# Optimization experiments

Measured on AMD Instinct MI355X. Metric: run time of the kernel, lower is better.

## Reference

```python
import jax, jax.numpy as jnp
import numpy as np

B, S, H = 2, 1024, 4096
NH, DH, NKV = 32, 128, 2          # heads, head_dim, kv groups
ROT = DH // 2                      # 64: GLM rotates first half of head dim
GROUP = NH // NKV                  # 16 query heads per kv group
SCALE = DH ** -0.5


def glm_rope(x, pos):
    """GLM interleaved rotary on first ROT dims. x: [B,S,h,DH], pos: [B,S] int."""
    rot, rest = x[..., :ROT], x[..., ROT:]
    inv_freq = 1.0 / (10000.0 ** (jnp.arange(0, ROT, 2, dtype=jnp.float32) / ROT))  # [ROT/2]
    ang = pos.astype(jnp.float32)[:, :, None] * inv_freq[None, None, :]             # [B,S,ROT/2]
    cos = jnp.cos(ang)[:, :, None, :]
    sin = jnp.sin(ang)[:, :, None, :]
    x0, x1 = rot[..., 0::2], rot[..., 1::2]
    o0 = x0 * cos - x1 * sin
    o1 = x1 * cos + x0 * sin
    rot_out = jnp.stack([o0, o1], axis=-1).reshape(rot.shape)
    return jnp.concatenate([rot_out, rest], axis=-1)


def setup_inputs() -> dict:
    key = jax.random.key(0)
    k1, k2, k3, k4 = jax.random.split(key, 4)
    return {
        "hidden_states": jax.random.normal(k1, (B, S, H), jnp.float32) * 0.02,
        "position_ids": jnp.arange(B * S, dtype=jnp.int32).reshape(B, S) % S,
        "W_qkv": jax.random.normal(k2, (H, NH * DH + 2 * NKV * DH), jnp.float32) * 0.02,
        "b_qkv": jax.random.normal(k3, (NH * DH + 2 * NKV * DH,), jnp.float32) * 0.02,
        "W_dense": jax.random.normal(k4, (NH * DH, H), jnp.float32) * 0.02,
    }


def reference(hidden_states, position_ids, W_qkv, b_qkv, W_dense):
    qkv = hidden_states @ W_qkv + b_qkv                              # [B,S,4608]
    q = qkv[..., : NH * DH].reshape(B, S, NH, DH)
    k = qkv[..., NH * DH : NH * DH + NKV * DH].reshape(B, S, NKV, DH)
    v = qkv[..., NH * DH + NKV * DH :].reshape(B, S, NKV, DH)

    q = glm_rope(q, position_ids)
    k = glm_rope(k, position_ids)

    # GQA: expand kv groups to all heads
    k = jnp.repeat(k, GROUP, axis=2)                                 # [B,S,NH,DH]
    v = jnp.repeat(v, GROUP, axis=2)

    scores = jnp.einsum("bqhd,bkhd->bhqk", q, k) * SCALE             # [B,NH,S,S]
    causal = jnp.tril(jnp.ones((S, S), dtype=bool))
    scores = jnp.where(causal[None, None], scores, jnp.finfo(scores.dtype).min)
    probs = jax.nn.softmax(scores, axis=-1)
    ctx = jnp.einsum("bhqk,bkhd->bqhd", probs, v).reshape(B, S, NH * DH)
    return ctx @ W_dense                                             # [B,S,H]
```

## Files before the change

kernel.cpp:

```cpp
#include <hip/hip_runtime.h>

#define B_    2
#define S_    1024
#define H_    4096
#define NH_   32
#define DH_   128
#define NKV_  2
#define GROUP_ 16
#define ROT_  64
#define NQKV_ 4608
#define SCALE_ 0.08838834764831845f
#define KVB   64

typedef __attribute__((ext_vector_type(8))) short bf16x8;
typedef __attribute__((ext_vector_type(4))) float f32x4;

typedef __attribute__((address_space(1))) const void* gptr_t;
typedef __attribute__((address_space(3))) void* lptr_t;

__device__ __forceinline__ unsigned short f2bf(float f) {
    unsigned int u = __builtin_bit_cast(unsigned int, f);
    u += 0x7FFFu + ((u >> 16) & 1u);
    return (unsigned short)(u >> 16);
}
__device__ __forceinline__ unsigned int pack2bf(float a, float b) {
    return (unsigned int)f2bf(a) | ((unsigned int)f2bf(b) << 16);
}

__global__ void k_f32_to_bf16(const float* __restrict__ in,
                              unsigned short* __restrict__ out, int n4) {
    int i = blockIdx.x * blockDim.x + threadIdx.x;
    if (i >= n4) return;
    const float4 v = reinterpret_cast<const float4*>(in)[i];
    ushort4 o;
    o.x = f2bf(v.x); o.y = f2bf(v.y); o.z = f2bf(v.z); o.w = f2bf(v.w);
    reinterpret_cast<ushort4*>(out)[i] = o;
}

__global__ void k_transpose_bf16(const float* __restrict__ in,
                                 unsigned short* __restrict__ out,
                                 int K, int N) {
    __shared__ float tile[32][33];
    const int n0 = blockIdx.x * 32, k0 = blockIdx.y * 32;
    const int tx = threadIdx.x, ty = threadIdx.y;
    for (int j = ty; j < 32; j += 8)
        tile[j][tx] = in[(size_t)(k0 + j) * N + n0 + tx];
    __syncthreads();
    for (int j = ty; j < 32; j += 8)
        out[(size_t)(n0 + j) * K + k0 + tx] = f2bf(tile[tx][j]);
}

__global__ void k_rope_tab(const int* __restrict__ pos_ids,
                           float2* __restrict__ tab) {
    const int idx = blockIdx.x * blockDim.x + threadIdx.x;
    if (idx >= B_ * S_ * 32) return;
    const int t = idx >> 5, pr = idx & 31;
    const float freq = exp2f(-0.41524101186092f * (float)pr);
    float sn, cs;
    sincosf((float)pos_ids[t] * freq, &sn, &cs);
    tab[idx] = make_float2(cs, sn);
}

template<int MODE>
__global__ __launch_bounds__(256, 2) void k_gemm(
    const unsigned short* __restrict__ A,
    const unsigned short* __restrict__ Bt,
    const float* __restrict__ bias,
    float* __restrict__ Cf,
    const float2* __restrict__ ctab,
    unsigned short* __restrict__ Qh,
    unsigned short* __restrict__ Kh,
    unsigned short* __restrict__ Vt,
    int M, int N, int K)
{
    __shared__ __align__(16) char lds[2][32768];

    const int tid  = threadIdx.x;
    const int wave = tid >> 6, lane = tid & 63;
    const int lrow = lane & 15, lhi = lane >> 4;
    const int wm = (wave >> 1) * 64, wn = (wave & 1) * 64;
    const size_t a_row0 = (size_t)blockIdx.y * 128;
    const size_t b_col0 = (size_t)blockIdx.x * 128;

    const size_t strideK = (size_t)K * 2;
    const char* Asrc = (const char*)A + (a_row0 + (tid >> 3)) * strideK;
    const char* Bsrc = (const char*)Bt + (b_col0 + (tid >> 3)) * strideK;
    const int swz_src = ((tid & 7) * 16) ^ (((tid >> 3) & 7) << 4);
    const int dst_off = tid * 16;

    f32x4 acc[4][4] = {};
    const int nt = K >> 6;

    #pragma unroll
    for (int j = 0; j < 4; j++) {
        __builtin_amdgcn_global_load_lds(
            (gptr_t)(Asrc + (size_t)j * 32 * strideK + swz_src),
            (lptr_t)(lds[0] + j * 4096 + dst_off), 16, 0, 0);
        __builtin_amdgcn_global_load_lds(
            (gptr_t)(Bsrc + (size_t)j * 32 * strideK + swz_src),
            (lptr_t)(lds[0] + 16384 + j * 4096 + dst_off), 16, 0, 0);
    }

    int cur = 0;
    for (int t = 0; t < nt; t++) {
        if (t + 1 < nt) {
            const size_t kb = (size_t)(t + 1) * 128;
            #pragma unroll
            for (int j = 0; j < 4; j++) {
                __builtin_amdgcn_global_load_lds(
                    (gptr_t)(Asrc + (size_t)j * 32 * strideK + kb + swz_src),
                    (lptr_t)(lds[cur ^ 1] + j * 4096 + dst_off), 16, 0, 0);
                __builtin_amdgcn_global_load_lds(
                    (gptr_t)(Bsrc + (size_t)j * 32 * strideK + kb + swz_src),
                    (lptr_t)(lds[cur ^ 1] + 16384 + j * 4096 + dst_off), 16, 0, 0);
            }
            asm volatile("s_waitcnt vmcnt(8)" ::: "memory");
        } else {
            asm volatile("s_waitcnt vmcnt(0)" ::: "memory");
        }
        __builtin_amdgcn_s_barrier();

        const char* La = lds[cur];
        const char* Lb = lds[cur] + 16384;
        bf16x8 af[4][2], bfr[4][2];
        #pragma unroll
        for (int i = 0; i < 4; i++) {
            const int fr = wm + i * 16 + lrow;
            af[i][0] = *(const bf16x8*)(La + fr * 128 + ((lhi * 16) ^ ((fr & 7) << 4)));
            af[i][1] = *(const bf16x8*)(La + fr * 128 + ((64 + lhi * 16) ^ ((fr & 7) << 4)));
        }
        #pragma unroll
        for (int j = 0; j < 4; j++) {
            const int br = wn + j * 16 + lrow;
            bfr[j][0] = *(const bf16x8*)(Lb + br * 128 + ((lhi * 16) ^ ((br & 7) << 4)));
            bfr[j][1] = *(const bf16x8*)(Lb + br * 128 + ((64 + lhi * 16) ^ ((br & 7) << 4)));
        }
        #pragma unroll
        for (int i = 0; i < 4; i++)
            #pragma unroll
            for (int j = 0; j < 4; j++) {
                acc[i][j] = __builtin_amdgcn_mfma_f32_16x16x32_bf16(
                    af[i][0], bfr[j][0], acc[i][j], 0, 0, 0);
                acc[i][j] = __builtin_amdgcn_mfma_f32_16x16x32_bf16(
                    af[i][1], bfr[j][1], acc[i][j], 0, 0, 0);
            }
        __builtin_amdgcn_s_barrier();
        cur ^= 1;
    }

    if (MODE == 0) {
        #pragma unroll
        for (int i = 0; i < 4; i++)
            #pragma unroll
            for (int j = 0; j < 4; j++) {
                const size_t grow0 = a_row0 + wm + i * 16 + lhi * 4;
                const size_t gcol  = b_col0 + wn + j * 16 + lrow;
                const float bi = bias ? bias[gcol] : 0.f;
                #pragma unroll
                for (int r = 0; r < 4; r++)
                    Cf[(grow0 + r) * N + gcol] = acc[i][j][r] + bi;
            }
    } else {
        const int bx = (int)blockIdx.x;
        const size_t bb = a_row0 >> 10;
        if (bx >= 34) {
            const int g = bx - 34;
            #pragma unroll
            for (int i = 0; i < 4; i++)
                #pragma unroll
                for (int j = 0; j < 4; j++) {
                    const int dloc = wn + j * 16 + lrow;
                    const float bi = bias[b_col0 + dloc];
                    const size_t row0 = a_row0 + wm + i * 16 + lhi * 4;
                    unsigned short* dst =
                        Vt + ((bb * NKV_ + g) * DH_ + dloc) * S_ + (row0 & 1023);
                    *reinterpret_cast<uint2*>(dst) = make_uint2(
                        pack2bf(acc[i][j][0] + bi, acc[i][j][1] + bi),
                        pack2bf(acc[i][j][2] + bi, acc[i][j][3] + bi));
                }
        } else {
            unsigned short* lds_c = (unsigned short*)&lds[0][0];
            #pragma unroll
            for (int i = 0; i < 4; i++)
                #pragma unroll
                for (int j = 0; j < 4; j++) {
                    const int dloc = wn + j * 16 + lrow;
                    const float bi = bias[b_col0 + dloc];
                    const int rloc0 = wm + i * 16 + lhi * 4;
                    float v[4];
                    #pragma unroll
                    for (int r = 0; r < 4; r++) v[r] = acc[i][j][r] + bi;
                    if (dloc < 64) {
                        const int pr = dloc >> 1;
                        #pragma unroll
                        for (int r = 0; r < 4; r++) {
                            const float2 cs = ctab[(a_row0 + rloc0 + r) * 32 + pr];
                            const float partner = __shfl_xor(v[r], 1);
                            v[r] = (dloc & 1) ? (v[r] * cs.x + partner * cs.y)
                                              : (v[r] * cs.x - partner * cs.y);
                        }
                    }
                    #pragma unroll
                    for (int r = 0; r < 4; r++)
                        lds_c[(rloc0 + r) * 128 + dloc] = f2bf(v[r]);
                }
            __syncthreads();
            unsigned short* base = (bx < 32)
                ? Qh + ((bb * NH_ + bx) * S_ + (a_row0 & 1023)) * DH_
                : Kh + ((bb * NKV_ + (bx - 32)) * S_ + (a_row0 & 1023)) * DH_;
            const int off = tid * 64;
            #pragma unroll
            for (int c = 0; c < 8; c++)
                *reinterpret_cast<uint4*>(base + off + c * 8) =
                    *reinterpret_cast<const uint4*>(lds_c + off + c * 8);
        }
    }
}

__global__ __launch_bounds__(256) void k_attn(
    const unsigned short* __restrict__ Qh,
    const unsigned short* __restrict__ Kh,
    const unsigned short* __restrict__ Vt,
    unsigned short* __restrict__ ctx)
{
    __shared__ __align__(16) char lds_kt[2][16384];
    __shared__ __align__(16) char lds_vt[16384];
    __shared__ __align__(16) char lds_p[4][2048];

    const int tid  = threadIdx.x;
    const int wave = tid >> 6, lane = tid & 63;
    const int lrow = lane & 15, lhi = lane >> 4;
    char* myp = lds_p[wave];

    const int blk  = blockIdx.x;
    const int pair = blk & 7;
    const int h    = (blk >> 3) & 31;
    const int b    = blk >> 8;
    const int g    = h >> 4;

    const char* Kbase = (const char*)(Kh + (size_t)((b * NKV_ + g) * S_) * DH_);
    const char* Vbase = (const char*)(Vt + (size_t)((b * NKV_ + g) * DH_) * S_);

    const int kcol = lrow * 16;
    const int vrow_l = lane >> 3;
    const int vcol = (lane & 7) * 16;

    for (int half = 0; half < 2; half++) {
        const int qt = half ? (15 - pair) : pair;
        const int q0 = qt * 64 + wave * 16;
        const int ntiles = qt + 1;
        const int q_glob = q0 + lrow;

        #pragma unroll
        for (int i = 0; i < 4; i++) {
            const int ci = wave * 4 + i;
            const int r  = ci * 4 + lhi;
            __builtin_amdgcn_global_load_lds(
                (gptr_t)(Kbase + (size_t)r * 256 + (kcol ^ ((r & 7) << 4))),
                (lptr_t)(lds_kt[0] + ci * 1024), 16, 0, 0);
        }
        const unsigned short* Qp = Qh + ((size_t)((b * NH_ + h) * S_) + q0) * DH_;
        bf16x8 a_q[4];
        #pragma unroll
        for (int ks = 0; ks < 4; ks++)
            a_q[ks] = *(const bf16x8*)(Qp + (size_t)lrow * DH_ + ks * 32 + lhi * 8);
        asm volatile("s_waitcnt vmcnt(0)" ::: "memory");
        __builtin_amdgcn_s_barrier();

        float m_run = -1e30f, l_run = 0.f;
        f32x4 o_acc[8] = {};
        int cur = 0;

        for (int t = 0; t < ntiles; t++) {
            const bool has_next = (t + 1 < ntiles);
            #pragma unroll
            for (int i = 0; i < 4; i++) {
                const int ci = wave * 4 + i;
                const int r  = ci * 8 + vrow_l;
                __builtin_amdgcn_global_load_lds(
                    (gptr_t)(Vbase + (size_t)r * (S_ * 2) + t * (KVB * 2)
                             + (vcol ^ ((r & 7) << 4))),
                    (lptr_t)(lds_vt + ci * 1024), 16, 0, 0);
            }
            if (has_next) {
                const char* ksrc = Kbase + (size_t)(t + 1) * 16384;
                #pragma unroll
                for (int i = 0; i < 4; i++) {
                    const int ci = wave * 4 + i;
                    const int r  = ci * 4 + lhi;
                    __builtin_amdgcn_global_load_lds(
                        (gptr_t)(ksrc + (size_t)r * 256 + (kcol ^ ((r & 7) << 4))),
                        (lptr_t)(lds_kt[cur ^ 1] + ci * 1024), 16, 0, 0);
                }
            }
            f32x4 s_acc[4] = {};
            #pragma unroll
            for (int sub = 0; sub < 4; sub++) {
                const int r = sub * 16 + lrow;
                #pragma unroll
                for (int ks = 0; ks < 4; ks++) {
                    const bf16x8 a_k = *(const bf16x8*)(
                        lds_kt[cur] + r * 256 + ((ks * 64 + lhi * 16) ^ ((r & 7) << 4)));
                    s_acc[sub] = __builtin_amdgcn_mfma_f32_16x16x32_bf16(
                        a_k, a_q[ks], s_acc[sub], 0, 0, 0);
                }
            }
            float pv[16];
            float mx = -1e30f;
            if (!has_next) {
                #pragma unroll
                for (int sub = 0; sub < 4; sub++)
                    #pragma unroll
                    for (int r = 0; r < 4; r++) {
                        const int kvg = t * KVB + sub * 16 + lhi * 4 + r;
                        float sv = s_acc[sub][r] * SCALE_;
                        if (kvg > q_glob) sv = -1e30f;
                        pv[sub * 4 + r] = sv;
                        mx = fmaxf(mx, sv);
                    }
            } else {
                #pragma unroll
                for (int sub = 0; sub < 4; sub++)
                    #pragma unroll
                    for (int r = 0; r < 4; r++) {
                        const float sv = s_acc[sub][r] * SCALE_;
                        pv[sub * 4 + r] = sv;
                        mx = fmaxf(mx, sv);
                    }
            }
            mx = fmaxf(mx, __shfl_xor(mx, 16));
            mx = fmaxf(mx, __shfl_xor(mx, 32));
            const float mnew = fmaxf(m_run, mx);
            const float scale = __expf(m_run - mnew);
            m_run = mnew;
            float sm = 0.f;
            #pragma unroll
            for (int i = 0; i < 16; i++) {
                const float e = __expf(pv[i] - mnew);
                pv[i] = e;
                sm += e;
            }
            sm += __shfl_xor(sm, 16);
            sm += __shfl_xor(sm, 32);
            l_run = l_run * scale + sm;
            #pragma unroll
            for (int d = 0; d < 8; d++) {
                o_acc[d][0] *= scale; o_acc[d][1] *= scale;
                o_acc[d][2] *= scale; o_acc[d][3] *= scale;
            }
            #pragma unroll
            for (int sub = 0; sub < 4; sub++) {
                const int off = (lrow * 128 + sub * 32 + lhi * 8) ^ ((lrow & 7) << 4);
                *reinterpret_cast<uint2*>(myp + off) = make_uint2(
                    pack2bf(pv[sub * 4 + 0], pv[sub * 4 + 1]),
                    pack2bf(pv[sub * 4 + 2], pv[sub * 4 + 3]));
            }
            bf16x8 a_p[2];
            #pragma unroll
            for (int frag = 0; frag < 2; frag++) {
                const int off = (lrow * 128 + frag * 64 + lhi * 16) ^ ((lrow & 7) << 4);
                a_p[frag] = *reinterpret_cast<const bf16x8*>(myp + off);
            }
            if (has_next) asm volatile("s_waitcnt vmcnt(4)" ::: "memory");
            else          asm volatile("s_waitcnt vmcnt(0)" ::: "memory");
            __builtin_amdgcn_s_barrier();
            #pragma unroll
            for (int d = 0; d < 8; d++) {
                const int r = d * 16 + lrow;
                #pragma unroll
                for (int frag = 0; frag < 2; frag++) {
                    const bf16x8 a_v = *(const bf16x8*)(
                        lds_vt + r * 128 + ((frag * 64 + lhi * 16) ^ ((r & 7) << 4)));
                    o_acc[d] = __builtin_amdgcn_mfma_f32_16x16x32_bf16(
                        a_v, a_p[frag], o_acc[d], 0, 0, 0);
                }
            }
            asm volatile("s_waitcnt vmcnt(0)" ::: "memory");
            __builtin_amdgcn_s_barrier();
            cur ^= 1;
        }
        const float inv = 1.f / l_run;
        const size_t row = (size_t)b * S_ + q0 + lrow;
        #pragma unroll
        for (int d = 0; d < 8; d++) {
            unsigned short* dst = ctx + row * (NH_ * DH_) + h * DH_ + d * 16 + lhi * 4;
            *reinterpret_cast<uint2*>(dst) = make_uint2(
                pack2bf(o_acc[d][0] * inv, o_acc[d][1] * inv),
                pack2bf(o_acc[d][2] * inv, o_acc[d][3] * inv));
        }
    }
}

extern "C" void kernel_launch(void* const* d_in, const int* in_sizes, int n_in,
                              void* d_out, int out_size, void* d_ws, size_t ws_size,
                              hipStream_t stream)
{
    const float* hidden  = (const float*)d_in[0];
    const int*   pos_ids = (const int*)d_in[1];
    const float* W_qkv   = (const float*)d_in[2];
    const float* b_qkv   = (const float*)d_in[3];
    const float* W_dense = (const float*)d_in[4];
    float* out = (float*)d_out;

    char* ws = (char*)d_ws;
    unsigned short* Xbf = (unsigned short*)(ws);
    unsigned short* Wqt = (unsigned short*)(ws + 16777216);
    unsigned short* Wdt = (unsigned short*)(ws + 54525952);
    float2*         ctab= (float2*)        (ws + 88080384);
    unsigned short* Qh  = (unsigned short*)(ws + 125829120);
    unsigned short* Kh  = (unsigned short*)(ws + 142606336);
    unsigned short* Vt  = (unsigned short*)(ws + 143654912);
    unsigned short* Ctx = (unsigned short*)(ws + 144703488);

    const int M = B_ * S_;

    k_f32_to_bf16<<<(M * H_ / 4 + 255) / 256, 256, 0, stream>>>(hidden, Xbf, M * H_ / 4);
    k_rope_tab<<<(M * 32 + 255) / 256, 256, 0, stream>>>(pos_ids, ctab);
    dim3 tb(32, 8);
    k_transpose_bf16<<<dim3(NQKV_ / 32, H_ / 32), tb, 0, stream>>>(W_qkv, Wqt, H_, NQKV_);
    k_transpose_bf16<<<dim3(H_ / 32, H_ / 32), tb, 0, stream>>>(W_dense, Wdt, H_, H_);
    k_gemm<1><<<dim3(NQKV_ / 128, M / 128), 256, 0, stream>>>(
        Xbf, Wqt, b_qkv, nullptr, ctab, Qh, Kh, Vt, M, NQKV_, H_);
    k_attn<<<B_ * NH_ * 8, 256, 0, stream>>>(Qh, Kh, Vt, Ctx);
    k_gemm<0><<<dim3(H_ / 128, M / 128), 256, 0, stream>>>(
        Ctx, Wdt, nullptr, out, nullptr, nullptr, nullptr, nullptr, M, H_, H_);
}
```

Baseline: 294.4 us.

## Shrink GEMM tile to 64x128, remap blocks across XCDs, swizzle epilogue LDS

Both GEMMs now use 64x128 output tiles instead of 128x128. The grid becomes 1D, with a block-id remap that groups consecutive tiles by XCD (blockIdx & 7), and occupancy is raised to 3 blocks per CU with smaller LDS buffers. The aim is more blocks and better load balance across the 256 CUs, plus better L2 locality per XCD. The QK epilogue staging buffer also gains an XOR swizzle to cut LDS bank conflicts. The trade-off is lower arithmetic intensity per tile, since each B fragment is reused over half as many rows.

Result: slower. 318.5 us (+8.2%).

```diff
diff --git a/kernel.cpp b/kernel.cpp
--- a/kernel.cpp
+++ b/kernel.cpp
@@ -62,7 +62,7 @@
 }
 
 template<int MODE>
-__global__ __launch_bounds__(256, 2) void k_gemm(
+__global__ __launch_bounds__(256, 3) void k_gemm(
     const unsigned short* __restrict__ A,
     const unsigned short* __restrict__ Bt,
     const float* __restrict__ bias,
@@ -73,14 +73,19 @@
     unsigned short* __restrict__ Vt,
     int M, int N, int K)
 {
-    __shared__ __align__(16) char lds[2][32768];
+    __shared__ __align__(16) char lds[2][24576];
 
     const int tid  = threadIdx.x;
     const int wave = tid >> 6, lane = tid & 63;
     const int lrow = lane & 15, lhi = lane >> 4;
-    const int wm = (wave >> 1) * 64, wn = (wave & 1) * 64;
-    const size_t a_row0 = (size_t)blockIdx.y * 128;
-    const size_t b_col0 = (size_t)blockIdx.x * 128;
+    const int wm = (wave >> 1) * 32, wn = (wave & 1) * 64;
+
+    const int cpx = gridDim.x >> 3;
+    const int Lid = ((int)blockIdx.x & 7) * cpx + ((int)blockIdx.x >> 3);
+    const int bx = Lid >> 5;
+    const int by = Lid & 31;
+    const size_t a_row0 = (size_t)by * 64;
+    const size_t b_col0 = (size_t)bx * 128;
 
     const size_t strideK = (size_t)K * 2;
     const char* Asrc = (const char*)A + (a_row0 + (tid >> 3)) * strideK;
@@ -88,43 +93,45 @@
     const int swz_src = ((tid & 7) * 16) ^ (((tid >> 3) & 7) << 4);
     const int dst_off = tid * 16;
 
-    f32x4 acc[4][4] = {};
+    f32x4 acc[2][4] = {};
     const int nt = K >> 6;
 
     #pragma unroll
-    for (int j = 0; j < 4; j++) {
+    for (int j = 0; j < 2; j++)
         __builtin_amdgcn_global_load_lds(
             (gptr_t)(Asrc + (size_t)j * 32 * strideK + swz_src),
             (lptr_t)(lds[0] + j * 4096 + dst_off), 16, 0, 0);
+    #pragma unroll
+    for (int j = 0; j < 4; j++)
         __builtin_amdgcn_global_load_lds(
             (gptr_t)(Bsrc + (size_t)j * 32 * strideK + swz_src),
-            (lptr_t)(lds[0] + 16384 + j * 4096 + dst_off), 16, 0, 0);
-    }
+            (lptr_t)(lds[0] + 8192 + j * 4096 + dst_off), 16, 0, 0);
 
     int cur = 0;
     for (int t = 0; t < nt; t++) {
         if (t + 1 < nt) {
             const size_t kb = (size_t)(t + 1) * 128;
             #pragma unroll
-            for (int j = 0; j < 4; j++) {
+            for (int j = 0; j < 2; j++)
                 __builtin_amdgcn_global_load_lds(
                     (gptr_t)(Asrc + (size_t)j * 32 * strideK + kb + swz_src),
                     (lptr_t)(lds[cur ^ 1] + j * 4096 + dst_off), 16, 0, 0);
+            #pragma unroll
+            for (int j = 0; j < 4; j++)
                 __builtin_amdgcn_global_load_lds(
                     (gptr_t)(Bsrc + (size_t)j * 32 * strideK + kb + swz_src),
-                    (lptr_t)(lds[cur ^ 1] + 16384 + j * 4096 + dst_off), 16, 0, 0);
-            }
-            asm volatile("s_waitcnt vmcnt(8)" ::: "memory");
+                    (lptr_t)(lds[cur ^ 1] + 8192 + j * 4096 + dst_off), 16, 0, 0);
+            asm volatile("s_waitcnt vmcnt(6)" ::: "memory");
         } else {
             asm volatile("s_waitcnt vmcnt(0)" ::: "memory");
         }
         __builtin_amdgcn_s_barrier();
 
         const char* La = lds[cur];
-        const char* Lb = lds[cur] + 16384;
-        bf16x8 af[4][2], bfr[4][2];
-        #pragma unroll
-        for (int i = 0; i < 4; i++) {
+        const char* Lb = lds[cur] + 8192;
+        bf16x8 af[2][2], bfr[4][2];
+        #pragma unroll
+        for (int i = 0; i < 2; i++) {
             const int fr = wm + i * 16 + lrow;
             af[i][0] = *(const bf16x8*)(La + fr * 128 + ((lhi * 16) ^ ((fr & 7) << 4)));
             af[i][1] = *(const bf16x8*)(La + fr * 128 + ((64 + lhi * 16) ^ ((fr & 7) << 4)));
@@ -136,7 +143,7 @@
             bfr[j][1] = *(const bf16x8*)(Lb + br * 128 + ((64 + lhi * 16) ^ ((br & 7) << 4)));
         }
         #pragma unroll
-        for (int i = 0; i < 4; i++)
+        for (int i = 0; i < 2; i++)
             #pragma unroll
             for (int j = 0; j < 4; j++) {
                 acc[i][j] = __builtin_amdgcn_mfma_f32_16x16x32_bf16(
@@ -150,7 +157,7 @@
 
     if (MODE == 0) {
         #pragma unroll
-        for (int i = 0; i < 4; i++)
+        for (int i = 0; i < 2; i++)
             #pragma unroll
             for (int j = 0; j < 4; j++) {
                 const size_t grow0 = a_row0 + wm + i * 16 + lhi * 4;
@@ -161,12 +168,11 @@
                     Cf[(grow0 + r) * N + gcol] = acc[i][j][r] + bi;
             }
     } else {
-        const int bx = (int)blockIdx.x;
         const size_t bb = a_row0 >> 10;
         if (bx >= 34) {
             const int g = bx - 34;
             #pragma unroll
-            for (int i = 0; i < 4; i++)
+            for (int i = 0; i < 2; i++)
                 #pragma unroll
                 for (int j = 0; j < 4; j++) {
                     const int dloc = wn + j * 16 + lrow;
@@ -179,9 +185,9 @@
                         pack2bf(acc[i][j][2] + bi, acc[i][j][3] + bi));
                 }
         } else {
-            unsigned short* lds_c = (unsigned short*)&lds[0][0];
-            #pragma unroll
-            for (int i = 0; i < 4; i++)
+            char* lc = &lds[0][0];
+            #pragma unroll
+            for (int i = 0; i < 2; i++)
                 #pragma unroll
                 for (int j = 0; j < 4; j++) {
                     const int dloc = wn + j * 16 + lrow;
@@ -201,18 +207,24 @@
                         }
                     }
                     #pragma unroll
-                    for (int r = 0; r < 4; r++)
-                        lds_c[(rloc0 + r) * 128 + dloc] = f2bf(v[r]);
+                    for (int r = 0; r < 4; r++) {
+                        const int row = rloc0 + r;
+                        *(unsigned short*)(lc + row * 256 +
+                            ((dloc * 2) ^ ((row & 7) << 4))) = f2bf(v[r]);
+                    }
                 }
             __syncthreads();
             unsigned short* base = (bx < 32)
                 ? Qh + ((bb * NH_ + bx) * S_ + (a_row0 & 1023)) * DH_
                 : Kh + ((bb * NKV_ + (bx - 32)) * S_ + (a_row0 & 1023)) * DH_;
-            const int off = tid * 64;
-            #pragma unroll
-            for (int c = 0; c < 8; c++)
-                *reinterpret_cast<uint4*>(base + off + c * 8) =
-                    *reinterpret_cast<const uint4*>(lds_c + off + c * 8);
+            #pragma unroll
+            for (int c = 0; c < 4; c++) {
+                const int lin = tid * 64 + c * 16;
+                const int row = lin >> 8;
+                const int col = (lin & 255) ^ ((row & 7) << 4);
+                *reinterpret_cast<uint4*>((char*)base + lin) =
+                    *reinterpret_cast<const uint4*>(lc + row * 256 + col);
+            }
         }
     }
 }
@@ -419,9 +431,9 @@
     dim3 tb(32, 8);
     k_transpose_bf16<<<dim3(NQKV_ / 32, H_ / 32), tb, 0, stream>>>(W_qkv, Wqt, H_, NQKV_);
     k_transpose_bf16<<<dim3(H_ / 32, H_ / 32), tb, 0, stream>>>(W_dense, Wdt, H_, H_);
-    k_gemm<1><<<dim3(NQKV_ / 128, M / 128), 256, 0, stream>>>(
+    k_gemm<1><<<dim3((NQKV_ / 128) * (M / 64)), 256, 0, stream>>>(
         Xbf, Wqt, b_qkv, nullptr, ctab, Qh, Kh, Vt, M, NQKV_, H_);
     k_attn<<<B_ * NH_ * 8, 256, 0, stream>>>(Qh, Kh, Vt, Ctx);
-    k_gemm<0><<<dim3(H_ / 128, M / 128), 256, 0, stream>>>(
+    k_gemm<0><<<dim3((H_ / 128) * (M / 64)), 256, 0, stream>>>(
         Ctx, Wdt, nullptr, out, nullptr, nullptr, nullptr, nullptr, M, H_, H_);
 }
```

## Enlarge attention query tile to 128 rows, two 16-row groups per wave

Applied to the files above, without the earlier changes.

The attention kernel now gives each block one 128-row query tile instead of a pair of 64-row tiles, and each wave handles two 16-query groups. This halves K/V tile loads per query and doubles MFMA work per LDS K/V fragment read. It also adds launch_bounds(256,2) and a larger P buffer. In exchange, register pressure rises (two accumulator sets), and the loss of causal pair balancing may leave idle waves on diagonal tiles and uneven block lengths.

After: 307.3 us. 4.4% more time.

```diff
diff --git a/kernel.cpp b/kernel.cpp
--- a/kernel.cpp
+++ b/kernel.cpp
@@ -217,7 +217,7 @@
     }
 }
 
-__global__ __launch_bounds__(256) void k_attn(
+__global__ __launch_bounds__(256, 2) void k_attn(
     const unsigned short* __restrict__ Qh,
     const unsigned short* __restrict__ Kh,
     const unsigned short* __restrict__ Vt,
@@ -225,18 +225,18 @@
 {
     __shared__ __align__(16) char lds_kt[2][16384];
     __shared__ __align__(16) char lds_vt[16384];
-    __shared__ __align__(16) char lds_p[4][2048];
+    __shared__ __align__(16) char lds_p[4][4096];
 
     const int tid  = threadIdx.x;
     const int wave = tid >> 6, lane = tid & 63;
     const int lrow = lane & 15, lhi = lane >> 4;
     char* myp = lds_p[wave];
 
-    const int blk  = blockIdx.x;
-    const int pair = blk & 7;
-    const int h    = (blk >> 3) & 31;
-    const int b    = blk >> 8;
-    const int g    = h >> 4;
+    const int blk = blockIdx.x;
+    const int qt  = 7 - (blk & 7);
+    const int h   = (blk >> 3) & 31;
+    const int b   = blk >> 8;
+    const int g   = h >> 4;
 
     const char* Kbase = (const char*)(Kh + (size_t)((b * NKV_ + g) * S_) * DH_);
     const char* Vbase = (const char*)(Vt + (size_t)((b * NKV_ + g) * DH_) * S_);
@@ -245,55 +245,59 @@
     const int vrow_l = lane >> 3;
     const int vcol = (lane & 7) * 16;
 
-    for (int half = 0; half < 2; half++) {
-        const int qt = half ? (15 - pair) : pair;
-        const int q0 = qt * 64 + wave * 16;
-        const int ntiles = qt + 1;
-        const int q_glob = q0 + lrow;
-
+    const int q0w = qt * 128 + wave * 32;
+    const int ntiles = 2 * qt + 2;
+
+    #pragma unroll
+    for (int i = 0; i < 4; i++) {
+        const int ci = wave * 4 + i;
+        const int r  = ci * 4 + lhi;
+        __builtin_amdgcn_global_load_lds(
+            (gptr_t)(Kbase + (size_t)r * 256 + (kcol ^ ((r & 7) << 4))),
+            (lptr_t)(lds_kt[0] + ci * 1024), 16, 0, 0);
+    }
+    const unsigned short* Qp = Qh + ((size_t)((b * NH_ + h) * S_) + q0w) * DH_;
+    bf16x8 aq[2][4];
+    #pragma unroll
+    for (int qg = 0; qg < 2; qg++)
+        #pragma unroll
+        for (int ks = 0; ks < 4; ks++)
+            aq[qg][ks] = *(const bf16x8*)(
+                Qp + (size_t)(qg * 16 + lrow) * DH_ + ks * 32 + lhi * 8);
+    asm volatile("s_waitcnt vmcnt(0)" ::: "memory");
+    __builtin_amdgcn_s_barrier();
+
+    float m_run[2] = {-1e30f, -1e30f}, l_run[2] = {0.f, 0.f};
+    f32x4 o_acc[8][2] = {};
+    int cur = 0;
+
+    for (int t = 0; t < ntiles; t++) {
+        const bool has_next = (t + 1 < ntiles);
+        const int kv0 = t * KVB;
+        const bool active = (kv0 <= q0w + 31);
         #pragma unroll
         for (int i = 0; i < 4; i++) {
             const int ci = wave * 4 + i;
-            const int r  = ci * 4 + lhi;
+            const int r  = ci * 8 + vrow_l;
             __builtin_amdgcn_global_load_lds(
-                (gptr_t)(Kbase + (size_t)r * 256 + (kcol ^ ((r & 7) << 4))),
-                (lptr_t)(lds_kt[0] + ci * 1024), 16, 0, 0);
-        }
-        const unsigned short* Qp = Qh + ((size_t)((b * NH_ + h) * S_) + q0) * DH_;
-        bf16x8 a_q[4];
-        #pragma unroll
-        for (int ks = 0; ks < 4; ks++)
-            a_q[ks] = *(const bf16x8*)(Qp + (size_t)lrow * DH_ + ks * 32 + lhi * 8);
-        asm volatile("s_waitcnt vmcnt(0)" ::: "memory");
-        __builtin_amdgcn_s_barrier();
-
-        float m_run = -1e30f, l_run = 0.f;
-        f32x4 o_acc[8] = {};
-        int cur = 0;
-
-        for (int t = 0; t < ntiles; t++) {
-            const bool has_next = (t + 1 < ntiles);
+                (gptr_t)(Vbase + (size_t)r * (S_ * 2) + t * (KVB * 2)
+                         + (vcol ^ ((r & 7) << 4))),
+                (lptr_t)(lds_vt + ci * 1024), 16, 0, 0);
+        }
+        if (has_next) {
+            const char* ksrc = Kbase + (size_t)(t + 1) * 16384;
             #pragma unroll
             for (int i = 0; i < 4; i++) {
                 const int ci = wave * 4 + i;
-                const int r  = ci * 8 + vrow_l;
+                const int r  = ci * 4 + lhi;
                 __builtin_amdgcn_global_load_lds(
-                    (gptr_t)(Vbase + (size_t)r * (S_ * 2) + t * (KVB * 2)
-                             + (vcol ^ ((r & 7) << 4))),
-                    (lptr_t)(lds_vt + ci * 1024), 16, 0, 0);
-            }
-            if (has_next) {
-                const char* ksrc = Kbase + (size_t)(t + 1) * 16384;
-                #pragma unroll
-                for (int i = 0; i < 4; i++) {
-                    const int ci = wave * 4 + i;
-                    const int r  = ci * 4 + lhi;
-                    __builtin_amdgcn_global_load_lds(
-                        (gptr_t)(ksrc + (size_t)r * 256 + (kcol ^ ((r & 7) << 4))),
-                        (lptr_t)(lds_kt[cur ^ 1] + ci * 1024), 16, 0, 0);
-                }
-            }
-            f32x4 s_acc[4] = {};
+                    (gptr_t)(ksrc + (size_t)r * 256 + (kcol ^ ((r & 7) << 4))),
+                    (lptr_t)(lds_kt[cur ^ 1] + ci * 1024), 16, 0, 0);
+            }
+        }
+        bf16x8 a_p[2][2];
+        if (active) {
+            f32x4 s_acc[4][2] = {};
             #pragma unroll
             for (int sub = 0; sub < 4; sub++) {
                 const int r = sub * 16 + lrow;
@@ -301,69 +305,82 @@
                 for (int ks = 0; ks < 4; ks++) {
                     const bf16x8 a_k = *(const bf16x8*)(
                         lds_kt[cur] + r * 256 + ((ks * 64 + lhi * 16) ^ ((r & 7) << 4)));
-                    s_acc[sub] = __builtin_amdgcn_mfma_f32_16x16x32_bf16(
-                        a_k, a_q[ks], s_acc[sub], 0, 0, 0);
-                }
-            }
-            float pv[16];
-            float mx = -1e30f;
-            if (!has_next) {
-                #pragma unroll
-                for (int sub = 0; sub < 4; sub++)
+                    s_acc[sub][0] = __builtin_amdgcn_mfma_f32_16x16x32_bf16(
+                        a_k, aq[0][ks], s_acc[sub][0], 0, 0, 0);
+                    s_acc[sub][1] = __builtin_amdgcn_mfma_f32_16x16x32_bf16(
+                        a_k, aq[1][ks], s_acc[sub][1], 0, 0, 0);
+                }
+            }
+            const bool needmask = (kv0 + KVB - 1 > q0w);
+            #pragma unroll
+            for (int qg = 0; qg < 2; qg++) {
+                const int q_glob = q0w + qg * 16 + lrow;
+                float pv[16];
+                float mx = -1e30f;
+                if (needmask) {
                     #pragma unroll
-                    for (int r = 0; r < 4; r++) {
-                        const int kvg = t * KVB + sub * 16 + lhi * 4 + r;
-                        float sv = s_acc[sub][r] * SCALE_;
-                        if (kvg > q_glob) sv = -1e30f;
-                        pv[sub * 4 + r] = sv;
-                        mx = fmaxf(mx, sv);
-                    }
-            } else {
-                #pragma unroll
-                for (int sub = 0; sub < 4; sub++)
+                    for (int sub = 0; sub < 4; sub++)
+                        #pragma unroll
+                        for (int r = 0; r < 4; r++) {
+                            const int kvg = kv0 + sub * 16 + lhi * 4 + r;
+                            float sv = s_acc[sub][qg][r] * SCALE_;
+                            if (kvg > q_glob) sv = -1e30f;
+                            pv[sub * 4 + r] = sv;
+                            mx = fmaxf(mx, sv);
+                        }
+                } else {
                     #pragma unroll
-                    for (int r = 0; r < 4; r++) {
-                        const float sv = s_acc[sub][r] * SCALE_;
-                        pv[sub * 4 + r] = sv;
-                        mx = fmaxf(mx, sv);
-                    }
-            }
-            mx = fmaxf(mx, __shfl_xor(mx, 16));
-            mx = fmaxf(mx, __shfl_xor(mx, 32));
-            const float mnew = fmaxf(m_run, mx);
-            const float scale = __expf(m_run - mnew);
-            m_run = mnew;
-            float sm = 0.f;
-            #pragma unroll
-            for (int i = 0; i < 16; i++) {
-                const float e = __expf(pv[i] - mnew);
-                pv[i] = e;
-                sm += e;
-            }
-            sm += __shfl_xor(sm, 16);
-            sm += __shfl_xor(sm, 32);
-            l_run = l_run * scale + sm;
-            #pragma unroll
-            for (int d = 0; d < 8; d++) {
-                o_acc[d][0] *= scale; o_acc[d][1] *= scale;
-                o_acc[d][2] *= scale; o_acc[d][3] *= scale;
-            }
-            #pragma unroll
-            for (int sub = 0; sub < 4; sub++) {
-                const int off = (lrow * 128 + sub * 32 + lhi * 8) ^ ((lrow & 7) << 4);
-                *reinterpret_cast<uint2*>(myp + off) = make_uint2(
-                    pack2bf(pv[sub * 4 + 0], pv[sub * 4 + 1]),
-                    pack2bf(pv[sub * 4 + 2], pv[sub * 4 + 3]));
-            }
-            bf16x8 a_p[2];
-            #pragma unroll
-            for (int frag = 0; frag < 2; frag++) {
-                const int off = (lrow * 128 + frag * 64 + lhi * 16) ^ ((lrow & 7) << 4);
-                a_p[frag] = *reinterpret_cast<const bf16x8*>(myp + off);
-            }
-            if (has_next) asm volatile("s_waitcnt vmcnt(4)" ::: "memory");
-            else          asm volatile("s_waitcnt vmcnt(0)" ::: "memory");
-            __builtin_amdgcn_s_barrier();
+                    for (int sub = 0; sub < 4; sub++)
+                        #pragma unroll
+                        for (int r = 0; r < 4; r++) {
+                            const float sv = s_acc[sub][qg][r] * SCALE_;
+                            pv[sub * 4 + r] = sv;
+                            mx = fmaxf(mx, sv);
+                        }
+                }
+                mx = fmaxf(mx, __shfl_xor(mx, 16));
+                mx = fmaxf(mx, __shfl_xor(mx, 32));
+                const float mnew = fmaxf(m_run[qg], mx);
+                const float scale = __expf(m_run[qg] - mnew);
+                m_run[qg] = mnew;
+                float sm = 0.f;
+                #pragma unroll
+                for (int i = 0; i < 16; i++) {
+                    const float e = __expf(pv[i] - mnew);
+                    pv[i] = e;
+                    sm += e;
+                }
+                sm += __shfl_xor(sm, 16);
+                sm += __shfl_xor(sm, 32);
+                l_run[qg] = l_run[qg] * scale + sm;
+                #pragma unroll
+                for (int d = 0; d < 8; d++) {
+                    o_acc[d][qg][0] *= scale; o_acc[d][qg][1] *= scale;
+                    o_acc[d][qg][2] *= scale; o_acc[d][qg][3] *= scale;
+                }
+                const int qrow = qg * 16 + lrow;
+                #pragma unroll
+                for (int sub = 0; sub < 4; sub++) {
+                    const int off = (qrow * 128 + sub * 32 + lhi * 8) ^ ((qrow & 7) << 4);
+                    *reinterpret_cast<uint2*>(myp + off) = make_uint2(
+                        pack2bf(pv[sub * 4 + 0], pv[sub * 4 + 1]),
+                        pack2bf(pv[sub * 4 + 2], pv[sub * 4 + 3]));
+                }
+            }
+            #pragma unroll
+            for (int qg = 0; qg < 2; qg++) {
+                const int qrow = qg * 16 + lrow;
+                #pragma unroll
+                for (int frag = 0; frag < 2; frag++) {
+                    const int off = (qrow * 128 + frag * 64 + lhi * 16) ^ ((qrow & 7) << 4);
+                    a_p[qg][frag] = *reinterpret_cast<const bf16x8*>(myp + off);
+                }
+            }
+        }
+        if (has_next) asm volatile("s_waitcnt vmcnt(4)" ::: "memory");
+        else          asm volatile("s_waitcnt vmcnt(0)" ::: "memory");
+        __builtin_amdgcn_s_barrier();
+        if (active) {
             #pragma unroll
             for (int d = 0; d < 8; d++) {
                 const int r = d * 16 + lrow;
@@ -371,22 +388,27 @@
                 for (int frag = 0; frag < 2; frag++) {
                     const bf16x8 a_v = *(const bf16x8*)(
                         lds_vt + r * 128 + ((frag * 64 + lhi * 16) ^ ((r & 7) << 4)));
-                    o_acc[d] = __builtin_amdgcn_mfma_f32_16x16x32_bf16(
-                        a_v, a_p[frag], o_acc[d], 0, 0, 0);
-                }
-            }
-            asm volatile("s_waitcnt vmcnt(0)" ::: "memory");
-            __builtin_amdgcn_s_barrier();
-            cur ^= 1;
-        }
-        const float inv = 1.f / l_run;
-        const size_t row = (size_t)b * S_ + q0 + lrow;
+                    o_acc[d][0] = __builtin_amdgcn_mfma_f32_16x16x32_bf16(
+                        a_v, a_p[0][frag], o_acc[d][0], 0, 0, 0);
+                    o_acc[d][1] = __builtin_amdgcn_mfma_f32_16x16x32_bf16(
+                        a_v, a_p[1][frag], o_acc[d][1], 0, 0, 0);
+                }
+            }
+        }
+        asm volatile("s_waitcnt vmcnt(0)" ::: "memory");
+        __builtin_amdgcn_s_barrier();
+        cur ^= 1;
+    }
+    #pragma unroll
+    for (int qg = 0; qg < 2; qg++) {
+        const float inv = 1.f / l_run[qg];
+        const size_t row = (size_t)b * S_ + q0w + qg * 16 + lrow;
         #pragma unroll
         for (int d = 0; d < 8; d++) {
             unsigned short* dst = ctx + row * (NH_ * DH_) + h * DH_ + d * 16 + lhi * 4;
             *reinterpret_cast<uint2*>(dst) = make_uint2(
-                pack2bf(o_acc[d][0] * inv, o_acc[d][1] * inv),
-                pack2bf(o_acc[d][2] * inv, o_acc[d][3] * inv));
+                pack2bf(o_acc[d][qg][0] * inv, o_acc[d][qg][1] * inv),
+                pack2bf(o_acc[d][qg][2] * inv, o_acc[d][qg][3] * inv));
         }
     }
 }
```
